# Kernel optimization log

Hardware: AMD Instinct MI355X
Metric: run time of the kernel (lower is better)

The kernel has to match this reference:

```python
import jax, jax.numpy as jnp
import numpy as np
from jax import lax

B, T, H = 4096, 2048, 32


def setup_inputs() -> dict:
    key = jax.random.key(0)
    ks = jax.random.split(key, 10)
    s = 1.0 / np.sqrt(H)  # PyTorch LSTM/Linear init scale
    x = jax.random.normal(ks[0], (B, T, 1), dtype=jnp.float32)
    lengths = jax.random.randint(ks[1], (B,), 1, T + 1, dtype=jnp.int32)
    u = lambda k, shape, sc: jax.random.uniform(k, shape, jnp.float32, -sc, sc)
    return {
        "x": x,
        "lengths": lengths,
        # backward-direction LSTM weights (only h_n[-1] is used by the head)
        "w_ih": u(ks[2], (4 * H, 1), s),
        "w_hh": u(ks[3], (4 * H, H), s),
        "b_ih": u(ks[4], (4 * H,), s),
        "b_hh": u(ks[5], (4 * H,), s),
        "fc_w": u(ks[6], (64, H), 1.0 / np.sqrt(H)),
        "fc_b": u(ks[7], (64,), 1.0 / np.sqrt(H)),
        "fc2_w": u(ks[8], (1, 64), 1.0 / np.sqrt(64)),
        "fc2_b": u(ks[9], (1,), 1.0 / np.sqrt(64)),
    }


def _backward_lstm_final(x, lengths, w_ih, w_hh, b_ih, b_hh):
    """Final hidden state of the backward direction of a packed BiLSTM.

    The backward direction reads each sequence from t=len-1 down to t=0 with
    zero initial state. Equivalently: scan padded x in reverse time order and
    only update (h, c) where t < length (packed-sequence semantics).
    """
    Bv, Tv, _ = x.shape
    ts = jnp.arange(Tv - 1, -1, -1)                       # reversed time indices
    xs_t = jnp.transpose(x[:, ::-1, :], (1, 0, 2))        # [T, B, 1]
    mask_t = ts[:, None] < lengths[None, :]               # [T, B]

    def step(carry, inp):
        h, c = carry
        xt, m = inp                                        # [B,1], [B]
        gates = xt @ w_ih.T + b_ih + h @ w_hh.T + b_hh     # [B, 4H]
        i, f, g, o = jnp.split(gates, 4, axis=-1)
        i = jax.nn.sigmoid(i)
        f = jax.nn.sigmoid(f)
        g = jnp.tanh(g)
        o = jax.nn.sigmoid(o)
        c_new = f * c + i * g
        h_new = o * jnp.tanh(c_new)
        mm = m[:, None]
        return (jnp.where(mm, h_new, h), jnp.where(mm, c_new, c)), None

    h0 = jnp.zeros((Bv, H), dtype=x.dtype)
    c0 = jnp.zeros((Bv, H), dtype=x.dtype)
    (h_n, _), _ = lax.scan(step, (h0, c0), (xs_t, mask_t))
    return h_n                                             # [B, H]


def reference(x, lengths, w_ih, w_hh, b_ih, b_hh, fc_w, fc_b, fc2_w, fc2_b):
    h_n = _backward_lstm_final(x, lengths, w_ih, w_hh, b_ih, b_hh)
    out = jax.nn.elu(h_n @ fc_w.T + fc_b)                  # [B, 64]
    out = jax.nn.sigmoid(out @ fc2_w.T + fc2_b)            # [B, 1]
    return out
```

## Files before the change

kernel.cpp:

```cpp
#include <hip/hip_runtime.h>

constexpr int BB = 4096;
constexpr int TT = 2048;
constexpr int HH = 32;
constexpr int GE = 16;

typedef float v2f __attribute__((ext_vector_type(2)));
typedef float v4f __attribute__((ext_vector_type(4)));
typedef float f32x4 __attribute__((ext_vector_type(4)));
typedef _Float16 f16x8 __attribute__((ext_vector_type(8)));
typedef _Float16 v8h __attribute__((ext_vector_type(8)));

__device__ __forceinline__ float fexp2(float x) { return __builtin_amdgcn_exp2f(x); }
__device__ __forceinline__ float frcp(float x)  { return __builtin_amdgcn_rcpf(x); }
__device__ __forceinline__ float fsigmoid(float x) {
    return frcp(1.0f + fexp2(x * -1.4426950408889634f));
}
__device__ __forceinline__ float felu(float x) {
    return x > 0.0f ? x : (fexp2(x * 1.4426950408889634f) - 1.0f);
}

__global__ void sort_by_len_kernel(const int* __restrict__ lengths, int* __restrict__ perm) {
    __shared__ int hist[TT];
    __shared__ int csum[256];
    const int tid = threadIdx.x;
    for (int i = tid; i < TT; i += 256) hist[i] = 0;
    __syncthreads();
    for (int i = tid; i < BB; i += 256) atomicAdd(&hist[TT - lengths[i]], 1);
    __syncthreads();
    const int base = tid * 8;
    int loc[8];
    int s = 0;
#pragma unroll
    for (int j = 0; j < 8; ++j) { loc[j] = hist[base + j]; s += loc[j]; }
    csum[tid] = s;
    __syncthreads();
    for (int off = 1; off < 256; off <<= 1) {
        int v = (tid >= off) ? csum[tid - off] : 0;
        __syncthreads();
        csum[tid] += v;
        __syncthreads();
    }
    int run = csum[tid] - s;
#pragma unroll
    for (int j = 0; j < 8; ++j) { int t = loc[j]; hist[base + j] = run; run += t; }
    __syncthreads();
    for (int i = tid; i < BB; i += 256) {
        int pos = atomicAdd(&hist[TT - lengths[i]], 1);
        perm[pos] = i;
    }
}

__global__ __attribute__((amdgpu_flat_work_group_size(512, 512)))
void lstm_kernel(const float* __restrict__ x, const int* __restrict__ lengths,
                 const float* __restrict__ w_ih, const float* __restrict__ w_hh,
                 const float* __restrict__ b_ih, const float* __restrict__ b_hh,
                 const float* __restrict__ fc_w, const float* __restrict__ fc_b,
                 const float* __restrict__ fc2_w, const float* __restrict__ fc2_b,
                 float* __restrict__ out, const int* __restrict__ perm) {
    __shared__ __align__(16) _Float16 hb[2][GE][40];
    __shared__ __align__(16) float xls[GE][68];
    __shared__ int barr[GE];
    __shared__ int Llds[GE];
    __shared__ int maxLs;

    const int tid  = threadIdx.x;
    const int wv   = tid >> 6;
    const int lane = tid & 63;
    const int lg   = lane >> 4;
    const int e    = lane & 15;

    const int g = blockIdx.x;
    if (tid < GE) {
        const int b = perm ? perm[GE * g + tid] : (GE * g + tid);
        barr[tid] = b;
        Llds[tid] = lengths[b];
    }
    for (int i = tid; i < 2 * GE * 40; i += 512) ((_Float16*)hb)[i] = (_Float16)0.0f;
    __syncthreads();
    if (tid == 0) {
        int m = 0;
        for (int i = 0; i < GE; ++i) m = max(m, Llds[i]);
        maxLs = m;
    }
    __syncthreads();
    const int maxL = maxLs;
    const int Lme  = Llds[e];

    const float NL2E = -1.4426950408889634f;

    const int r  = lane & 15;
    const int sg = r & 3;
    const int ua = 4 * wv + (r >> 2);
    const float asc = (sg == 2) ? 2.0f * NL2E : NL2E;
    f16x8 afr;
    {
        const v4f* wp = reinterpret_cast<const v4f*>(w_hh + (sg * 32 + ua) * 32 + 8 * lg);
        const v4f wa = wp[0], wb = wp[1];
        afr = (f16x8){(_Float16)(wa.x * asc), (_Float16)(wa.y * asc),
                      (_Float16)(wa.z * asc), (_Float16)(wa.w * asc),
                      (_Float16)(wb.x * asc), (_Float16)(wb.y * asc),
                      (_Float16)(wb.z * asc), (_Float16)(wb.w * asc)};
    }
    const int ud = 4 * wv + lg;
    float wih_[4], bs_[4];
#pragma unroll
    for (int i = 0; i < 4; ++i) {
        const float scd = (i == 2) ? 2.0f * NL2E : NL2E;
        wih_[i] = w_ih[i * 32 + ud] * scd;
        bs_[i]  = (b_ih[i * 32 + ud] + b_hh[i * 32 + ud]) * scd;
    }

    float c = 0.0f;
    int p = 0;

    for (int s = maxL - 1; s >= 0; --s) {
        if (s == maxL - 1 || (s & 63) == 63) {
            const int tb = s & ~63;
            const int es = tid >> 5, j2 = (tid & 31) * 2;
            const float* xp = x + (size_t)barr[es] * TT + tb + j2;
            *reinterpret_cast<v2f*>(&xls[es][j2]) = *reinterpret_cast<const v2f*>(xp);
            __syncthreads();
        }
        const f16x8 bf = *reinterpret_cast<const f16x8*>(&hb[p][e][lg * 8]);
        const float xe = xls[e][s & 63];
        f32x4 C;
#pragma unroll
        for (int i = 0; i < 4; ++i) C[i] = fmaf(wih_[i], xe, bs_[i]);
        const f32x4 D = __builtin_amdgcn_mfma_f32_16x16x32_f16(afr, bf, C, 0, 0, 0);
        const bool act = (s < Lme);

        const float Ei = fexp2(D[0]), Ef = fexp2(D[1]);
        const float Eg = fexp2(D[2]), Eo = fexp2(D[3]);
        const float R1 = frcp((1.0f + Ei) * (1.0f + Eg));
        const float ig = (1.0f - Eg) * R1;
        const float R2 = frcp((1.0f + Ef) * (1.0f + Eo));
        const float sf = (1.0f + Eo) * R2;
        const float so = (1.0f + Ef) * R2;
        const float cn = fmaf(sf, c, ig);
        c = act ? cn : c;
        const float tc = 1.0f - 2.0f * frcp(1.0f + fexp2(c * 2.8853900817779268f));
        const float hn = act ? (so * tc) : 0.0f;

        hb[p ^ 1][e][ud] = (_Float16)hn;
        __syncthreads();
        p ^= 1;
    }

    for (int e2 = 2 * wv; e2 < 2 * wv + 2; ++e2) {
        float hf[32];
        const v8h* hp8 = reinterpret_cast<const v8h*>(&hb[p][e2][0]);
#pragma unroll
        for (int q4 = 0; q4 < 4; ++q4) {
            const v8h hh = hp8[q4];
#pragma unroll
            for (int j = 0; j < 8; ++j) hf[8 * q4 + j] = (float)hh[j];
        }
        float a = fc_b[lane];
        const v4f* fp = reinterpret_cast<const v4f*>(fc_w + lane * 32);
#pragma unroll
        for (int q4 = 0; q4 < 8; ++q4) {
            const v4f f = fp[q4];
            a = fmaf(f.x, hf[4 * q4 + 0], a);
            a = fmaf(f.y, hf[4 * q4 + 1], a);
            a = fmaf(f.z, hf[4 * q4 + 2], a);
            a = fmaf(f.w, hf[4 * q4 + 3], a);
        }
        float partial = felu(a) * fc2_w[lane];
#pragma unroll
        for (int m = 32; m >= 1; m >>= 1) partial += __shfl_xor(partial, m, 64);
        if (lane == 0) out[barr[e2]] = fsigmoid(partial + fc2_b[0]);
    }
}

extern "C" void kernel_launch(void* const* d_in, const int* in_sizes, int n_in,
                              void* d_out, int out_size, void* d_ws, size_t ws_size,
                              hipStream_t stream) {
    const float* x       = (const float*)d_in[0];
    const int*   lengths = (const int*)d_in[1];
    const float* w_ih    = (const float*)d_in[2];
    const float* w_hh    = (const float*)d_in[3];
    const float* b_ih    = (const float*)d_in[4];
    const float* b_hh    = (const float*)d_in[5];
    const float* fc_w    = (const float*)d_in[6];
    const float* fc_b    = (const float*)d_in[7];
    const float* fc2_w   = (const float*)d_in[8];
    const float* fc2_b   = (const float*)d_in[9];
    float* out = (float*)d_out;

    int* perm = nullptr;
    if (ws_size >= (size_t)BB * sizeof(int)) {
        perm = (int*)d_ws;
        hipLaunchKernelGGL(sort_by_len_kernel, dim3(1), dim3(256), 0, stream, lengths, perm);
    }
    hipLaunchKernelGGL(lstm_kernel, dim3(BB / GE), dim3(512), 0, stream,
                       x, lengths, w_ih, w_hh, b_ih, b_hh,
                       fc_w, fc_b, fc2_w, fc2_b, out, perm);
}
```

Baseline: 614.6 us.

## Double-buffer x staging with register prefetch and LDS-only barrier waits

Input x chunks are now double-buffered in shared memory. The next 64-step chunk is prefetched into registers one chunk ahead, which removes the extra barrier and the exposed global load every 64 steps. The per-step __syncthreads is replaced by an s_waitcnt lgkmcnt(0) plus s_barrier, so in-flight global prefetches are not waited on. x values are read from LDS as float4 every four steps, and maxL is computed per thread to drop a setup barrier. In exchange the code relies on hand-written waitcnt and barrier ordering, and the logic is more complex.

Measured after the change: 749.9 us. 22.0% more time.

```diff
diff --git a/kernel.cpp b/kernel.cpp
--- a/kernel.cpp
+++ b/kernel.cpp
@@ -59,10 +59,9 @@
                  const float* __restrict__ fc2_w, const float* __restrict__ fc2_b,
                  float* __restrict__ out, const int* __restrict__ perm) {
     __shared__ __align__(16) _Float16 hb[2][GE][40];
-    __shared__ __align__(16) float xls[GE][68];
+    __shared__ __align__(16) float xls[2][GE][68];
     __shared__ int barr[GE];
     __shared__ int Llds[GE];
-    __shared__ int maxLs;
 
     const int tid  = threadIdx.x;
     const int wv   = tid >> 6;
@@ -78,14 +77,10 @@
     }
     for (int i = tid; i < 2 * GE * 40; i += 512) ((_Float16*)hb)[i] = (_Float16)0.0f;
     __syncthreads();
-    if (tid == 0) {
-        int m = 0;
-        for (int i = 0; i < GE; ++i) m = max(m, Llds[i]);
-        maxLs = m;
-    }
-    __syncthreads();
-    const int maxL = maxLs;
-    const int Lme  = Llds[e];
+    int maxL = 0;
+#pragma unroll
+    for (int i = 0; i < GE; ++i) maxL = max(maxL, Llds[i]);
+    const int Lme = Llds[e];
 
     const float NL2E = -1.4426950408889634f;
 
@@ -114,16 +109,32 @@
     float c = 0.0f;
     int p = 0;
 
-    for (int s = maxL - 1; s >= 0; --s) {
-        if (s == maxL - 1 || (s & 63) == 63) {
-            const int tb = s & ~63;
-            const int es = tid >> 5, j2 = (tid & 31) * 2;
-            const float* xp = x + (size_t)barr[es] * TT + tb + j2;
-            *reinterpret_cast<v2f*>(&xls[es][j2]) = *reinterpret_cast<const v2f*>(xp);
-            __syncthreads();
-        }
+    const int es = tid >> 5;
+    const int j2 = (tid & 31) * 2;
+    const float* xbase = x + (size_t)barr[es] * TT + j2;
+
+    int s = maxL - 1;
+    const int tb0 = s & ~63;
+    {
+        const v2f xr = *reinterpret_cast<const v2f*>(xbase + tb0);
+        *reinterpret_cast<v2f*>(&xls[0][es][j2]) = xr;
+    }
+    int qx = 0;
+    v2f xpref = (v2f)(0.0f);
+    if (tb0 >= 64) xpref = *reinterpret_cast<const v2f*>(xbase + tb0 - 64);
+    asm volatile("s_waitcnt lgkmcnt(0)" ::: "memory");
+    __builtin_amdgcn_s_barrier();
+    asm volatile("" ::: "memory");
+
+    v4f x4 = (v4f)(0.0f);
+    for (; s >= 0; --s) {
+        const int sl = s & 63;
+        if ((s & 3) == 3 || s == maxL - 1) {
+            x4 = *reinterpret_cast<const v4f*>(&xls[qx][e][sl & ~3]);
+        }
+        const float xe = x4[s & 3];
+
         const f16x8 bf = *reinterpret_cast<const f16x8*>(&hb[p][e][lg * 8]);
-        const float xe = xls[e][s & 63];
         f32x4 C;
 #pragma unroll
         for (int i = 0; i < 4; ++i) C[i] = fmaf(wih_[i], xe, bs_[i]);
@@ -143,7 +154,16 @@
         const float hn = act ? (so * tc) : 0.0f;
 
         hb[p ^ 1][e][ud] = (_Float16)hn;
-        __syncthreads();
+
+        if (sl == 0 && s > 0) {
+            *reinterpret_cast<v2f*>(&xls[qx ^ 1][es][j2]) = xpref;
+            if (s >= 128)
+                xpref = *reinterpret_cast<const v2f*>(xbase + s - 128);
+            qx ^= 1;
+        }
+        asm volatile("s_waitcnt lgkmcnt(0)" ::: "memory");
+        __builtin_amdgcn_s_barrier();
+        asm volatile("" ::: "memory");
         p ^= 1;
     }
 
```
